# Performance work log

Measured on AMD Instinct MI355X. Metric: run time of the kernel, lower is better.

## Reference

```python
import jax, jax.numpy as jnp
import numpy as np

NEG_CLAMP = -100.0  # torch F.binary_cross_entropy clamps log terms at -100


def _ccl_labels(fg):
    """4-connectivity connected-component labeling of a [H,W] bool mask.
    Labels are assigned in raster-scan first-encounter order, matching
    scipy.ndimage.label with the default structure. Background = 0.
    Implemented as min-index label propagation to a fixed point: each
    component ends up tagged with the min flat index of its pixels (its
    first raster-scan pixel), then roots are ranked by cumsum to get 1..num.
    """
    H, W = fg.shape
    INF = H * W  # sentinel larger than any flat index
    idx = jnp.arange(INF, dtype=jnp.int32).reshape(H, W)
    init = jnp.where(fg, idx, INF)

    def step(x):
        up = jnp.concatenate([x[1:], jnp.full((1, W), INF, x.dtype)], axis=0)
        down = jnp.concatenate([jnp.full((1, W), INF, x.dtype), x[:-1]], axis=0)
        left = jnp.concatenate([x[:, 1:], jnp.full((H, 1), INF, x.dtype)], axis=1)
        right = jnp.concatenate([jnp.full((H, 1), INF, x.dtype), x[:, :-1]], axis=1)
        m = jnp.minimum(jnp.minimum(up, down), jnp.minimum(left, right))
        return jnp.where(fg, jnp.minimum(x, m), INF)

    def cond(carry):
        return carry[1]

    def body(carry):
        x, _ = carry
        nx = step(x)
        return nx, jnp.any(nx != x)

    x, _ = jax.lax.while_loop(cond, body, (init, jnp.array(True)))

    flat = x.reshape(-1)
    fgf = fg.reshape(-1)
    # a pixel is the root of its component iff its propagated tag == its own index
    is_root = fgf & (flat == jnp.arange(INF, dtype=jnp.int32))
    rank = jnp.cumsum(is_root.astype(jnp.int32))  # rank[r] = scipy label of root r
    labels = jnp.where(fgf, rank[jnp.clip(flat, 0, INF - 1)], 0)
    return labels.reshape(H, W)


def _target_map(fg):
    """Replicates: labels == labels.flatten()[1:].argmax() + 1 (faithful to source,
    including its quirky use of argmax position as the selected label value)."""
    labels = _ccl_labels(fg)
    lf = labels.reshape(-1)
    v = jnp.argmax(lf[1:]) + 1  # first occurrence of max, like numpy argmax
    return (labels == v).astype(jnp.float32)


def setup_inputs() -> dict:
    key = jax.random.key(0)
    pred = jax.random.uniform(key, (32, 1, 512, 512), dtype=jnp.float32)
    return {"pred": pred}


def reference(pred):
    fg = pred[:, 0] >= 0.5  # [N,H,W] bool
    target = jax.vmap(_target_map)(fg)[:, None]  # [N,1,H,W] float
    logp = jnp.maximum(jnp.log(pred), NEG_CLAMP)
    log1mp = jnp.maximum(jnp.log1p(-pred), NEG_CLAMP)
    return -jnp.mean(target * logp + (1.0 - target) * log1mp)
```

## Files before the change

kernel.cpp:

```cpp
#include <hip/hip_runtime.h>
#include <math.h>

#define IMG_W 512
#define IMG_H 512
#define HW (IMG_W * IMG_H)
#define LOGHW 18
#define NIMG 32
#define NTOT (NIMG * HW)
#define TILE 64
#define TPI 64
#define NTILE (NIMG * TPI)
#define CPI 64
#define NSCHUNK (NIMG * CPI)
#define VBORD ((8 - 1) * IMG_H)
#define BORD_PER_IMG (VBORD + (8 - 1) * IMG_W)
#define NBORD (NIMG * BORD_PER_IMG)

__device__ __forceinline__ void uf_unite(int* L, int a, int b) {
    while (true) {
        int p = ((volatile int*)L)[a];
        while (p != a) { a = p; p = ((volatile int*)L)[a]; }
        p = ((volatile int*)L)[b];
        while (p != b) { b = p; p = ((volatile int*)L)[b]; }
        if (a == b) return;
        if (a < b) { int t = a; a = b; b = t; }
        int old = atomicMin(&L[a], b);
        if (old == a) return;
        a = old;
    }
}

__global__ __launch_bounds__(256) void k_local(const float* __restrict__ pred,
                                               int* __restrict__ L,
                                               float* __restrict__ partials) {
    __shared__ int lab[TILE * TILE];
    __shared__ float sred[256];
    int tile = blockIdx.x;
    int img = tile >> 6;
    int t = tile & (TPI - 1);
    int ty = t >> 3, tx = t & 7;
    int baseLocal = (ty * TILE) * IMG_W + tx * TILE;
    const float* pi = pred + ((size_t)img << LOGHW);
    int* Li = L + ((size_t)img << LOGHW);
    int tid = threadIdx.x;
    int lane = tid & 63, wave = tid >> 6;

    float acc = 0.0f;
#pragma unroll
    for (int j = 0; j < 16; j++) {
        int row = wave + j * 4;
        float p = pi[baseLocal + row * IMG_W + lane];
        acc += fmaxf(log1pf(-p), -100.0f);
        bool fg = (p >= 0.5f);
        unsigned long long bal = __ballot(fg);
        unsigned long long starts = bal & ~(bal << 1);
        unsigned long long maskle =
            (lane == 63) ? ~0ULL : ((1ULL << (lane + 1)) - 1ULL);
        int lb = -1;
        if (fg) {
            unsigned long long pre = starts & maskle;
            int startLane = 63 - __builtin_clzll(pre);
            lb = row * TILE + startLane;
        }
        lab[row * TILE + lane] = lb;
    }
    __syncthreads();
#pragma unroll
    for (int j = 0; j < 16; j++) {
        int row = 1 + wave + j * 4;
        if (row > 63) break;
        int i = row * TILE + lane;
        bool c = (lab[i] >= 0) && (lab[i - TILE] >= 0);
        unsigned long long cb = __ballot(c);
        unsigned long long cs = cb & ~(cb << 1);
        if ((cs >> lane) & 1ULL) uf_unite(lab, i, i - TILE);
    }
    __syncthreads();
#pragma unroll
    for (int j = 0; j < 4; j++) {
        int i4 = (tid + j * 256) * 4;
        int ly = i4 >> 6, lx = i4 & 63;
        int4 o;
        int* op = (int*)&o;
#pragma unroll
        for (int k = 0; k < 4; k++) {
            int p = lab[i4 + k];
            if (p < 0) op[k] = -1;
            else {
                int x = i4 + k;
                while (p != x) { x = p; p = lab[x]; }
                op[k] = baseLocal + (x >> 6) * IMG_W + (x & 63);
            }
        }
        *(int4*)(Li + baseLocal + ly * IMG_W + lx) = o;
    }
    sred[tid] = acc;
    __syncthreads();
    for (int s = 128; s > 0; s >>= 1) {
        if (tid < s) sred[tid] += sred[tid + s];
        __syncthreads();
    }
    if (tid == 0) partials[blockIdx.x] = sred[0];
}

__global__ void k_border(int* __restrict__ L) {
    int gid = blockIdx.x * blockDim.x + threadIdx.x;
    if (gid >= NBORD) return;
    int img = gid / BORD_PER_IMG;
    int r = gid - img * BORD_PER_IMG;
    int* Li = L + ((size_t)img << LOGHW);
    int a, b;
    if (r < VBORD) {
        int k = r >> 9, y = r & 511;
        int x = k * TILE + (TILE - 1);
        a = y * IMG_W + x; b = a + 1;
    } else {
        int r2 = r - VBORD;
        int k = r2 >> 9, x = r2 & 511;
        int y = k * TILE + (TILE - 1);
        a = y * IMG_W + x; b = a + IMG_W;
    }
    if (Li[a] >= 0 && Li[b] >= 0) uf_unite(Li, a, b);
}

__global__ __launch_bounds__(256) void k_stats(const int* __restrict__ L,
                                               int* __restrict__ cntArr,
                                               int* __restrict__ maxArr,
                                               int* __restrict__ minArr) {
    __shared__ int s1[256], s2[256], s3[256];
    int chunk = blockIdx.x;
    int img = chunk >> 6;
    int baseL = (chunk & 63) * 4096;
    const int* Li = L + ((size_t)img << LOGHW);
    int t = threadIdx.x;
    int cnt = 0, mx = -1, mn = HW;
#pragma unroll
    for (int j = 0; j < 4; j++) {
        int off = baseL + (t + j * 256) * 4;
        int4 l4 = *(const int4*)(Li + off);
        const int* lp = (const int*)&l4;
#pragma unroll
        for (int k = 0; k < 4; k++) {
            int local = off + k;
            int p = lp[k];
            bool root = (p == local);
            cnt += root ? 1 : 0;
            if (root && local > mx) mx = local;
            if (p >= 0 && local >= 1 && local < mn) mn = local;
        }
    }
    s1[t] = cnt; s2[t] = mx; s3[t] = mn;
    __syncthreads();
    for (int s = 128; s > 0; s >>= 1) {
        if (t < s) {
            s1[t] += s1[t + s];
            s2[t] = max(s2[t], s2[t + s]);
            s3[t] = min(s3[t], s3[t + s]);
        }
        __syncthreads();
    }
    if (t == 0) { cntArr[chunk] = s1[0]; maxArr[chunk] = s2[0]; minArr[chunk] = s3[0]; }
}

__global__ __launch_bounds__(256) void k_rv(const int* __restrict__ cntArr,
                                            const int* __restrict__ maxArr,
                                            const int* __restrict__ minArr,
                                            const int* __restrict__ L,
                                            int* __restrict__ rv) {
    __shared__ int sc[256], sm[256], sn[256];
    __shared__ int sel_chunk, sel_base, result;
    int img = blockIdx.x, t = threadIdx.x;
    int cnt = (t < CPI) ? cntArr[img * CPI + t] : 0;
    sc[t] = cnt;
    sm[t] = (t < CPI) ? maxArr[img * CPI + t] : -1;
    sn[t] = (t < CPI) ? minArr[img * CPI + t] : HW;
    if (t == 0) result = -2;
    __syncthreads();
    for (int off = 1; off < 256; off <<= 1) {
        int v2 = (t >= off) ? sc[t - off] : 0;
        __syncthreads();
        sc[t] += v2;
        __syncthreads();
    }
    int num = sc[255];
    int inc = sc[t], exc = inc - cnt;
    for (int s = 128; s > 0; s >>= 1) {
        if (t < s) { sm[t] = max(sm[t], sm[t + s]); sn[t] = min(sn[t], sn[t + s]); }
        __syncthreads();
    }
    int last_root = sm[0], minFg = sn[0];
    int v;
    if (last_root >= 1) v = last_root;
    else if (last_root == 0) v = (minFg < HW) ? minFg : 1;
    else v = 1;
    if (v >= 1 && v <= num) {
        if (exc < v && v <= inc) { sel_chunk = t; sel_base = exc; }
        __syncthreads();
        int c = sel_chunk, base = sel_base;
        const int* Li = L + ((size_t)img << LOGHW);
        int baseL = c * 4096;
        int f[16];
        int sum = 0;
#pragma unroll
        for (int j = 0; j < 4; j++) {
            int off = baseL + t * 16 + j * 4;
            int4 l4 = *(const int4*)(Li + off);
            const int* lp = (const int*)&l4;
#pragma unroll
            for (int k = 0; k < 4; k++) {
                f[j * 4 + k] = (lp[k] == off + k) ? 1 : 0;
                sum += f[j * 4 + k];
            }
        }
        __syncthreads();
        sc[t] = sum;
        __syncthreads();
        for (int off = 1; off < 256; off <<= 1) {
            int v2 = (t >= off) ? sc[t - off] : 0;
            __syncthreads();
            sc[t] += v2;
            __syncthreads();
        }
        int exc2 = sc[t] - sum;
        int need = v - base;
        if (exc2 < need && need <= sc[t]) {
            int run = exc2;
#pragma unroll
            for (int k = 0; k < 16; k++) {
                run += f[k];
                if (run == need) { result = baseL + t * 16 + k; break; }
            }
        }
        __syncthreads();
    } else {
        __syncthreads();
    }
    if (t == 0) rv[img] = result;
}

__global__ __launch_bounds__(256) void k_loss(const float* __restrict__ pred,
                                              const int* __restrict__ L,
                                              const int* __restrict__ rvArr,
                                              float* __restrict__ partials2) {
    __shared__ float sred[256];
    int blk = blockIdx.x;
    int img = blk >> 6;
    int rvv = rvArr[img];
    if (rvv < 0) {
        if (threadIdx.x == 0) partials2[blk] = 0.0f;
        return;
    }
    const int* Li = L + ((size_t)img << LOGHW);
    int baseG = blk * 4096;
    int t = threadIdx.x;
    float acc = 0.0f;
#pragma unroll
    for (int j = 0; j < 4; j++) {
        int off = baseG + (t + j * 256) * 4;
        float4 p4 = *(const float4*)(pred + off);
        int4 l4 = *(const int4*)(L + off);
        const float* pp = (const float*)&p4;
        const int* lp = (const int*)&l4;
#pragma unroll
        for (int k = 0; k < 4; k++) {
            int p = lp[k];
            if (p < 0) continue;
            int x = p;
            int q = Li[x];
            while (q != x) { x = q; q = Li[x]; }
            if (x == rvv) {
                float pr = pp[k];
                float logp = fmaxf(logf(pr), -100.0f);
                float log1mp = fmaxf(log1pf(-pr), -100.0f);
                acc += logp - log1mp;
            }
        }
    }
    sred[t] = acc;
    __syncthreads();
    for (int s = 128; s > 0; s >>= 1) {
        if (t < s) sred[t] += sred[t + s];
        __syncthreads();
    }
    if (t == 0) partials2[blk] = sred[0];
}

__global__ __launch_bounds__(256) void k_final(const float* __restrict__ partials,
                                               const float* __restrict__ partials2,
                                               float* __restrict__ out) {
    __shared__ double s[256];
    int t = threadIdx.x;
    double acc = 0.0;
#pragma unroll
    for (int j = 0; j < 8; j++) {
        acc += (double)partials[t + j * 256] + (double)partials2[t + j * 256];
    }
    s[t] = acc;
    __syncthreads();
    for (int st = 128; st > 0; st >>= 1) {
        if (t < st) s[t] += s[t + st];
        __syncthreads();
    }
    if (t == 0) out[0] = (float)(-s[0] / (double)NTOT);
}

extern "C" void kernel_launch(void* const* d_in, const int* in_sizes, int n_in,
                              void* d_out, int out_size, void* d_ws, size_t ws_size,
                              hipStream_t stream) {
    const float* pred = (const float*)d_in[0];
    float* out = (float*)d_out;

    char* ws = (char*)d_ws;
    int* L = (int*)ws;
    int* cntArr = (int*)(ws + (size_t)NTOT * 4);
    int* maxArr = cntArr + NSCHUNK;
    int* minArr = maxArr + NSCHUNK;
    float* partials = (float*)(minArr + NSCHUNK);
    float* partials2 = partials + NTILE;
    int* rv = (int*)(partials2 + NTILE);

    dim3 b(256);
    k_local<<<dim3(NTILE), b, 0, stream>>>(pred, L, partials);
    k_border<<<dim3((NBORD + 255) / 256), b, 0, stream>>>(L);
    k_stats<<<dim3(NSCHUNK), b, 0, stream>>>(L, cntArr, maxArr, minArr);
    k_rv<<<dim3(NIMG), b, 0, stream>>>(cntArr, maxArr, minArr, L, rv);
    k_loss<<<dim3(NTILE), b, 0, stream>>>(pred, L, rv, partials2);
    k_final<<<1, b, 0, stream>>>(partials, partials2, out);
}
```

Before: 134.1 us.

## Move log1mp reduction into loss kernel, add path compression and ballot-deduped border unions

Moves the background log(1-p) accumulation out of the labeling kernel into the loss kernel, so one block reduction and one partials array are dropped and the final reduction reads a single buffer. Adds path halving in the shared-memory label flattening. Border unions are now deduplicated with a wave ballot so only run starts call union-find. Also switches to the fast __logf intrinsics and removes the bounds check in the border kernel (NBORD is a multiple of 256), which may slightly change accuracy.

```diff
diff --git a/kernel.cpp b/kernel.cpp
--- a/kernel.cpp
+++ b/kernel.cpp
@@ -31,10 +31,8 @@
 }
 
 __global__ __launch_bounds__(256) void k_local(const float* __restrict__ pred,
-                                               int* __restrict__ L,
-                                               float* __restrict__ partials) {
+                                               int* __restrict__ L) {
     __shared__ int lab[TILE * TILE];
-    __shared__ float sred[256];
     int tile = blockIdx.x;
     int img = tile >> 6;
     int t = tile & (TPI - 1);
@@ -45,12 +43,10 @@
     int tid = threadIdx.x;
     int lane = tid & 63, wave = tid >> 6;
 
-    float acc = 0.0f;
 #pragma unroll
     for (int j = 0; j < 16; j++) {
         int row = wave + j * 4;
         float p = pi[baseLocal + row * IMG_W + lane];
-        acc += fmaxf(log1pf(-p), -100.0f);
         bool fg = (p >= 0.5f);
         unsigned long long bal = __ballot(fg);
         unsigned long long starts = bal & ~(bal << 1);
@@ -84,28 +80,25 @@
         int* op = (int*)&o;
 #pragma unroll
         for (int k = 0; k < 4; k++) {
-            int p = lab[i4 + k];
+            int x = i4 + k;
+            int p = lab[x];
             if (p < 0) op[k] = -1;
             else {
-                int x = i4 + k;
-                while (p != x) { x = p; p = lab[x]; }
+                while (p != x) {
+                    int g = lab[p];
+                    lab[x] = g;
+                    x = g;
+                    p = lab[x];
+                }
                 op[k] = baseLocal + (x >> 6) * IMG_W + (x & 63);
             }
         }
         *(int4*)(Li + baseLocal + ly * IMG_W + lx) = o;
     }
-    sred[tid] = acc;
-    __syncthreads();
-    for (int s = 128; s > 0; s >>= 1) {
-        if (tid < s) sred[tid] += sred[tid + s];
-        __syncthreads();
-    }
-    if (tid == 0) partials[blockIdx.x] = sred[0];
 }
 
 __global__ void k_border(int* __restrict__ L) {
     int gid = blockIdx.x * blockDim.x + threadIdx.x;
-    if (gid >= NBORD) return;
     int img = gid / BORD_PER_IMG;
     int r = gid - img * BORD_PER_IMG;
     int* Li = L + ((size_t)img << LOGHW);
@@ -120,7 +113,10 @@
         int y = k * TILE + (TILE - 1);
         a = y * IMG_W + x; b = a + IMG_W;
     }
-    if (Li[a] >= 0 && Li[b] >= 0) uf_unite(Li, a, b);
+    bool c = (Li[a] >= 0) && (Li[b] >= 0);
+    unsigned long long cb = __ballot(c);
+    unsigned long long cs = cb & ~(cb << 1);
+    if ((cs >> (threadIdx.x & 63)) & 1ULL) uf_unite(Li, a, b);
 }
 
 __global__ __launch_bounds__(256) void k_stats(const int* __restrict__ L,
@@ -241,38 +237,45 @@
 __global__ __launch_bounds__(256) void k_loss(const float* __restrict__ pred,
                                               const int* __restrict__ L,
                                               const int* __restrict__ rvArr,
-                                              float* __restrict__ partials2) {
+                                              float* __restrict__ partials) {
     __shared__ float sred[256];
     int blk = blockIdx.x;
     int img = blk >> 6;
     int rvv = rvArr[img];
-    if (rvv < 0) {
-        if (threadIdx.x == 0) partials2[blk] = 0.0f;
-        return;
-    }
-    const int* Li = L + ((size_t)img << LOGHW);
     int baseG = blk * 4096;
     int t = threadIdx.x;
     float acc = 0.0f;
-#pragma unroll
-    for (int j = 0; j < 4; j++) {
-        int off = baseG + (t + j * 256) * 4;
-        float4 p4 = *(const float4*)(pred + off);
-        int4 l4 = *(const int4*)(L + off);
-        const float* pp = (const float*)&p4;
-        const int* lp = (const int*)&l4;
-#pragma unroll
-        for (int k = 0; k < 4; k++) {
-            int p = lp[k];
-            if (p < 0) continue;
-            int x = p;
-            int q = Li[x];
-            while (q != x) { x = q; q = Li[x]; }
-            if (x == rvv) {
+    if (rvv < 0) {
+#pragma unroll
+        for (int j = 0; j < 4; j++) {
+            int off = baseG + (t + j * 256) * 4;
+            float4 p4 = *(const float4*)(pred + off);
+            const float* pp = (const float*)&p4;
+#pragma unroll
+            for (int k = 0; k < 4; k++)
+                acc += fmaxf(__logf(1.0f - pp[k]), -100.0f);
+        }
+    } else {
+        const int* Li = L + ((size_t)img << LOGHW);
+#pragma unroll
+        for (int j = 0; j < 4; j++) {
+            int off = baseG + (t + j * 256) * 4;
+            float4 p4 = *(const float4*)(pred + off);
+            int4 l4 = *(const int4*)(L + off);
+            const float* pp = (const float*)&p4;
+            const int* lp = (const int*)&l4;
+#pragma unroll
+            for (int k = 0; k < 4; k++) {
                 float pr = pp[k];
-                float logp = fmaxf(logf(pr), -100.0f);
-                float log1mp = fmaxf(log1pf(-pr), -100.0f);
-                acc += logp - log1mp;
+                float log1mp = fmaxf(__logf(1.0f - pr), -100.0f);
+                acc += log1mp;
+                int p = lp[k];
+                if (p >= 0) {
+                    int x = p, q = Li[x];
+                    while (q != x) { x = q; q = Li[x]; }
+                    if (x == rvv)
+                        acc += fmaxf(__logf(pr), -100.0f) - log1mp;
+                }
             }
         }
     }
@@ -282,19 +285,16 @@
         if (t < s) sred[t] += sred[t + s];
         __syncthreads();
     }
-    if (t == 0) partials2[blk] = sred[0];
+    if (t == 0) partials[blk] = sred[0];
 }
 
 __global__ __launch_bounds__(256) void k_final(const float* __restrict__ partials,
-                                               const float* __restrict__ partials2,
                                                float* __restrict__ out) {
     __shared__ double s[256];
     int t = threadIdx.x;
     double acc = 0.0;
 #pragma unroll
-    for (int j = 0; j < 8; j++) {
-        acc += (double)partials[t + j * 256] + (double)partials2[t + j * 256];
-    }
+    for (int j = 0; j < 8; j++) acc += (double)partials[t + j * 256];
     s[t] = acc;
     __syncthreads();
     for (int st = 128; st > 0; st >>= 1) {
@@ -316,14 +316,13 @@
     int* maxArr = cntArr + NSCHUNK;
     int* minArr = maxArr + NSCHUNK;
     float* partials = (float*)(minArr + NSCHUNK);
-    float* partials2 = partials + NTILE;
-    int* rv = (int*)(partials2 + NTILE);
+    int* rv = (int*)(partials + NSCHUNK);
 
     dim3 b(256);
-    k_local<<<dim3(NTILE), b, 0, stream>>>(pred, L, partials);
-    k_border<<<dim3((NBORD + 255) / 256), b, 0, stream>>>(L);
+    k_local<<<dim3(NTILE), b, 0, stream>>>(pred, L);
+    k_border<<<dim3(NBORD / 256), b, 0, stream>>>(L);
     k_stats<<<dim3(NSCHUNK), b, 0, stream>>>(L, cntArr, maxArr, minArr);
     k_rv<<<dim3(NIMG), b, 0, stream>>>(cntArr, maxArr, minArr, L, rv);
-    k_loss<<<dim3(NTILE), b, 0, stream>>>(pred, L, rv, partials2);
-    k_final<<<1, b, 0, stream>>>(partials, partials2, out);
-}
+    k_loss<<<dim3(NSCHUNK), b, 0, stream>>>(pred, L, rv, partials);
+    k_final<<<1, b, 0, stream>>>(partials, out);
+}
```

After: 124.5 us. -7.2%, faster.
